# Kernel optimization log

Hardware: AMD Instinct MI355X
Metric: run time of the kernel (lower is better)

The kernel has to match this reference:

```python
import jax, jax.numpy as jnp
import numpy as np

TOKENS, D_MODEL, VOCAB = 8192, 1024, 32000


def setup_inputs() -> dict:
    key = jax.random.key(0)
    k1, k2, k3 = jax.random.split(key, 3)
    inp = jax.random.normal(k1, (TOKENS, D_MODEL), dtype=jnp.float32)
    proj_weight = jax.random.normal(k2, (VOCAB, D_MODEL), dtype=jnp.float32) * 0.02
    target = jax.random.randint(k3, (TOKENS,), 0, VOCAB, dtype=jnp.int64)
    return {"input": inp, "proj_weight": proj_weight, "target": target}


def reference(input, proj_weight, target):
    # Fused linear -> log_softmax -> NLL with reduction='sum'.
    # Original tiles over tokens/vocab with an online max/sum; the math is
    # exactly: loss = sum_t ( logsumexp_v(logits[t, :]) - logits[t, target[t]] )
    # with max/sum/target-score reductions done in float32 (fp_max/fp_sum/fp_target=True).
    logits = jnp.matmul(input, proj_weight.T).astype(jnp.float32)  # [tokens, vocab]
    lse = jax.nn.logsumexp(logits, axis=1)                          # [tokens]
    target_score = jnp.take_along_axis(logits, target[:, None].astype(jnp.int32), axis=1)[:, 0]
    return jnp.sum(lse - target_score)  # scalar, reduction='sum'
```

## Files before the change

kernel.cpp:

```cpp
#include <hip/hip_runtime.h>
#include <stdint.h>


#define TOKENS 8192
#define DMODEL 1024
#define VOCAB  32000

#define NBM32  (TOKENS / 128)
#define NBN32  (VOCAB / 256)
#define NWG32  (NBM32 * NBN32)

#define NBM    (TOKENS / 128)
#define NBN    (VOCAB / 128)
#define NWG    (NBM * NBN)
#define CHUNK  (NWG / 8)

typedef float  f32x4   __attribute__((ext_vector_type(4)));
typedef float  f32x16  __attribute__((ext_vector_type(16)));
typedef int    i32x8   __attribute__((ext_vector_type(8)));
typedef __bf16 bf16x8  __attribute__((ext_vector_type(8)));
typedef unsigned short u16;
typedef u16 u16x4 __attribute__((ext_vector_type(4)));

__device__ __forceinline__ u16 f2bf(float f) {
  union { float f; uint32_t u; } v; v.f = f;
  return (u16)((v.u + 0x7FFFu + ((v.u >> 16) & 1u)) >> 16);
}

__device__ __forceinline__ uint8_t f2e4m3(float x) {
  union { float f; uint32_t u; } v; v.f = x;
  const uint32_t s = (v.u >> 24) & 0x80u;
  const float ax = fabsf(x);
  if (ax >= 464.f) return (uint8_t)(s | 0x7E);
  if (ax < 0.015625f) {
    const int q = (int)rintf(ax * 512.f);
    return (uint8_t)(s | (uint32_t)q);
  }
  uint32_t u = v.u;
  u += 0x000FFFFFu + ((u >> 20) & 1u);
  const int E = (int)((u >> 23) & 0xFF) - 127;
  const uint32_t m3 = (u >> 20) & 0x7u;
  return (uint8_t)(s | (uint32_t)(((E + 7) << 3) | m3));
}

__device__ __forceinline__ void g2lds16(const void* gsrc, void* ldst) {
  __builtin_amdgcn_global_load_lds(
      (const __attribute__((address_space(1))) uint32_t*)(uintptr_t)gsrc,
      (__attribute__((address_space(3))) uint32_t*)(uintptr_t)ldst,
      16, 0, 0);
}

__global__ void convert_fp8_tiled(const float* __restrict__ in, uint8_t* __restrict__ out,
                                  long long total, int NR, int log2ts, float scale) {
  const long long step = (long long)gridDim.x * blockDim.x * 8;
  for (long long d = ((long long)blockIdx.x * blockDim.x + threadIdx.x) * 8;
       d < total; d += step) {
    const long long tile = d >> log2ts;
    const int x  = (int)(d & ((1 << log2ts) - 1));
    const int sub = x >> 11;
    const int l   = (x >> 5) & 63;
    const int b0  = x & 31;
    const int rb  = (int)(tile >> 4);
    const int kt  = (int)(tile & 15);
    const int row = rb * NR + sub * 32 + (l & 31);
    const int k   = kt * 64 + (l >> 5) * 32 + b0;
    const float* src = in + (size_t)row * DMODEL + k;
    const float4 f0 = *(const float4*)src;
    const float4 f1 = *(const float4*)(src + 4);
    uint8_t r[8] = { f2e4m3(f0.x * scale), f2e4m3(f0.y * scale),
                     f2e4m3(f0.z * scale), f2e4m3(f0.w * scale),
                     f2e4m3(f1.x * scale), f2e4m3(f1.y * scale),
                     f2e4m3(f1.z * scale), f2e4m3(f1.w * scale) };
    *(uint64_t*)(out + d) = *(const uint64_t*)r;
  }
}

template <int NCHUNK>
__device__ __forceinline__ void stage_lin(const uint8_t* __restrict__ src, uint8_t* dst,
                                          int wave, int lane) {
#pragma unroll
  for (int p = 0; p < NCHUNK / 4; ++p) {
    const int c = p * 4 + wave;
    g2lds16(src + c * 1024 + lane * 16, (void*)(dst + c * 1024));
  }
}

__device__ __forceinline__ void kstep32(const uint8_t* As, const uint8_t* Bs,
                                        f32x16 (&acc)[2][4],
                                        int wr, int wc, int lane) {
  i32x8 a[2], b[4];
  const uint8_t* ap = As + (wr * 2) * 2048 + lane * 32;
#pragma unroll
  for (int mi = 0; mi < 2; ++mi) {
    *(uint4*)&a[mi]       = *(const uint4*)(ap + mi * 2048);
    *((uint4*)&a[mi] + 1) = *(const uint4*)(ap + mi * 2048 + 16);
  }
  const uint8_t* bp = Bs + (wc * 4) * 2048 + lane * 32;
#pragma unroll
  for (int ni = 0; ni < 4; ++ni) {
    *(uint4*)&b[ni]       = *(const uint4*)(bp + ni * 2048);
    *((uint4*)&b[ni] + 1) = *(const uint4*)(bp + ni * 2048 + 16);
  }
  __builtin_amdgcn_s_setprio(1);
#pragma unroll
  for (int mi = 0; mi < 2; ++mi)
#pragma unroll
    for (int ni = 0; ni < 4; ++ni)
      acc[mi][ni] = __builtin_amdgcn_mfma_scale_f32_32x32x64_f8f6f4(
          a[mi], b[ni], acc[mi][ni], 0, 0,
          0, 0x7F7F7F7F, 0, 0x7F7F7F7F);
  __builtin_amdgcn_s_setprio(0);
}

__global__ __launch_bounds__(256, 2)
void gemm_lse_fp8v2(const uint8_t* __restrict__ A8, const uint8_t* __restrict__ B8,
                    float* __restrict__ S) {
  __shared__ uint8_t smem[49152];
  uint8_t* A0 = smem;
  uint8_t* B0 = smem + 8192;
  uint8_t* A1 = smem + 24576;
  uint8_t* B1 = smem + 32768;

  const int tid  = threadIdx.x;
  const int lane = tid & 63;
  const int wave = tid >> 6;
  const int wr = wave >> 1, wc = wave & 1;

  const int lid  = blockIdx.x;
  const int band = lid & 7;
  const int idx2 = lid >> 3;
  const int bn   = idx2 >> 3;
  const int bm   = band * 8 + (idx2 & 7);
  const int arow = bm * 128;

  const uint8_t* Abase = A8 + (size_t)(bm * 16) * 8192;
  const uint8_t* Bbase = B8 + (size_t)(bn * 16) * 16384;

  f32x16 acc[2][4];
#pragma unroll
  for (int mi = 0; mi < 2; ++mi)
#pragma unroll
    for (int ni = 0; ni < 4; ++ni) acc[mi][ni] = (f32x16)(0.f);

  stage_lin<8>(Abase, A0, wave, lane);
  stage_lin<16>(Bbase, B0, wave, lane);

#pragma unroll 1
  for (int tt = 0; tt < 8; ++tt) {
    const int t0 = 2 * tt;
    __syncthreads();
    if (t0 + 1 < 16) {
      stage_lin<8>(Abase + (size_t)(t0 + 1) * 8192, A1, wave, lane);
      stage_lin<16>(Bbase + (size_t)(t0 + 1) * 16384, B1, wave, lane);
    }
    kstep32(A0, B0, acc, wr, wc, lane);
    __syncthreads();
    if (t0 + 2 < 16) {
      stage_lin<8>(Abase + (size_t)(t0 + 2) * 8192, A0, wave, lane);
      stage_lin<16>(Bbase + (size_t)(t0 + 2) * 16384, B0, wave, lane);
    }
    kstep32(A1, B1, acc, wr, wc, lane);
  }

#pragma unroll
  for (int mi = 0; mi < 2; ++mi) {
#pragma unroll
    for (int r = 0; r < 16; ++r) {
      float v = 0.f;
#pragma unroll
      for (int ni = 0; ni < 4; ++ni) v += __expf(acc[mi][ni][r] * 0.0625f);
      v += __shfl_xor(v, 1);
      v += __shfl_xor(v, 2);
      v += __shfl_xor(v, 4);
      v += __shfl_xor(v, 8);
      v += __shfl_xor(v, 16);
      if ((lane & 31) == 0) {
        const int row = arow + (wr * 2 + mi) * 32 + (r & 3) + 8 * (r >> 2) + 4 * (lane >> 5);
        atomicAdd(&S[row], v);
      }
    }
  }
}

__global__ __launch_bounds__(256)
void gemm_lse_fb(const float* __restrict__ Af, const float* __restrict__ Bf,
                 float* __restrict__ S) {
  __shared__ u16 As[128 * 64];
  __shared__ u16 Bs[128 * 64];

  const int tid  = threadIdx.x;
  const int lane = tid & 63;
  const int wave = tid >> 6;
  const int wr = wave >> 1, wc = wave & 1;
  const int l15 = lane & 15, l4 = lane >> 4;

  const int lid = blockIdx.x;
  const int wid = (lid & 7) * CHUNK + (lid >> 3);
  const int bm = wid & (NBM - 1);
  const int bn = wid / NBM;

  f32x4 acc[4][4];
#pragma unroll
  for (int m = 0; m < 4; ++m)
#pragma unroll
    for (int n = 0; n < 4; ++n) acc[m][n] = (f32x4)(0.f);

  for (int kt = 0; kt < DMODEL / 64; ++kt) {
    const int k0 = kt * 64;
    {
      const int row = tid >> 4;
      const int kq  = (tid & 15) * 4;
#pragma unroll
      for (int r = 0; r < 8; ++r) {
        const int rr = r * 16 + row;
        const int kd = kq ^ ((rr & 7) << 3);
        float4 a4 = *(const float4*)(Af + (size_t)(bm * 128 + rr) * DMODEL + k0 + kq);
        float4 b4 = *(const float4*)(Bf + (size_t)(bn * 128 + rr) * DMODEL + k0 + kq);
        u16x4 ap = { f2bf(a4.x), f2bf(a4.y), f2bf(a4.z), f2bf(a4.w) };
        u16x4 bp = { f2bf(b4.x), f2bf(b4.y), f2bf(b4.z), f2bf(b4.w) };
        *(u16x4*)&As[rr * 64 + kd] = ap;
        *(u16x4*)&Bs[rr * 64 + kd] = bp;
      }
    }
    __syncthreads();
#pragma unroll
    for (int kk = 0; kk < 2; ++kk) {
      bf16x8 av[4], bv[4];
      const int swz = (l15 & 7) << 3;
      const int kc  = (kk * 32 + l4 * 8) ^ swz;
#pragma unroll
      for (int m = 0; m < 4; ++m)
        av[m] = *(const bf16x8*)&As[(wr * 64 + m * 16 + l15) * 64 + kc];
#pragma unroll
      for (int n = 0; n < 4; ++n)
        bv[n] = *(const bf16x8*)&Bs[(wc * 64 + n * 16 + l15) * 64 + kc];
#pragma unroll
      for (int m = 0; m < 4; ++m)
#pragma unroll
        for (int n = 0; n < 4; ++n)
          acc[m][n] = __builtin_amdgcn_mfma_f32_16x16x32_bf16(av[m], bv[n], acc[m][n], 0, 0, 0);
    }
    __syncthreads();
  }

#pragma unroll
  for (int m = 0; m < 4; ++m) {
#pragma unroll
    for (int j = 0; j < 4; ++j) {
      float v = 0.f;
#pragma unroll
      for (int n = 0; n < 4; ++n) v += __expf(acc[m][n][j]);
      v += __shfl_xor(v, 1);
      v += __shfl_xor(v, 2);
      v += __shfl_xor(v, 4);
      v += __shfl_xor(v, 8);
      if (l15 == 0) {
        const int row = bm * 128 + wr * 64 + m * 16 + l4 * 4 + j;
        atomicAdd(&S[row], v);
      }
    }
  }
}

__global__ void target_score_k(const float* __restrict__ inp, const float* __restrict__ W,
                               const int* __restrict__ tgt, float* __restrict__ ts) {
  const int gtid = blockIdx.x * blockDim.x + threadIdx.x;
  const int t = gtid >> 6;
  const int lane = threadIdx.x & 63;
  if (t >= TOKENS) return;
  bool allhi0 = true, anylo = false;
  for (int i = 0; i < 64; ++i) {
    if (tgt[2 * i + 1] != 0) allhi0 = false;
    if (tgt[2 * i] != 0) anylo = true;
  }
  const int v = (allhi0 && anylo) ? tgt[2 * t] : tgt[t];
  const float4* xr = (const float4*)(inp + (size_t)t * DMODEL);
  const float4* wr = (const float4*)(W + (size_t)v * DMODEL);
  float s = 0.f;
#pragma unroll
  for (int i = 0; i < 4; ++i) {
    float4 a = xr[lane + 64 * i];
    float4 b = wr[lane + 64 * i];
    s += a.x * b.x + a.y * b.y + a.z * b.z + a.w * b.w;
  }
#pragma unroll
  for (int off = 32; off >= 1; off >>= 1) s += __shfl_xor(s, off);
  if (lane == 0) ts[t] = s;
}

__global__ void finalize_k(const float* __restrict__ S, const float* __restrict__ ts,
                           float* __restrict__ out) {
  __shared__ float red[16];
  float s = 0.f;
  for (int t = threadIdx.x; t < TOKENS; t += blockDim.x) s += __logf(S[t]) - ts[t];
#pragma unroll
  for (int off = 32; off >= 1; off >>= 1) s += __shfl_xor(s, off);
  const int wave = threadIdx.x >> 6, lane = threadIdx.x & 63;
  if (lane == 0) red[wave] = s;
  __syncthreads();
  if (threadIdx.x == 0) {
    float tot = 0.f;
    for (int w = 0; w < (int)(blockDim.x >> 6); ++w) tot += red[w];
    out[0] = tot;
  }
}

extern "C" void kernel_launch(void* const* d_in, const int* in_sizes, int n_in,
                              void* d_out, int out_size, void* d_ws, size_t ws_size,
                              hipStream_t stream) {
  const float* inp = (const float*)d_in[0];
  const float* W   = (const float*)d_in[1];
  const int*   tgt = (const int*)d_in[2];
  float* out = (float*)d_out;

  char* ws = (char*)d_ws;
  float* S  = (float*)ws;
  float* ts = (float*)(ws + 32 * 1024);
  const size_t offA = 64 * 1024;
  const long long totalA = (long long)TOKENS * DMODEL;
  const long long totalB = (long long)VOCAB * DMODEL;
  const size_t offB = offA + (size_t)totalA;
  const size_t need = offB + (size_t)totalB;
  const bool preconv = ws_size >= need;

  hipMemsetAsync(S, 0, TOKENS * sizeof(float), stream);

  if (preconv) {
    uint8_t* A8 = (uint8_t*)(ws + offA);
    uint8_t* B8 = (uint8_t*)(ws + offB);
    convert_fp8_tiled<<<4096, 256, 0, stream>>>(inp, A8, totalA, 128, 13, 1.0f);
    convert_fp8_tiled<<<16000, 256, 0, stream>>>(W, B8, totalB, 256, 14, 16.0f);
    gemm_lse_fp8v2<<<NWG32, 256, 0, stream>>>(A8, B8, S);
  } else {
    gemm_lse_fb<<<NWG, 256, 0, stream>>>(inp, W, S);
  }
  target_score_k<<<(TOKENS * 64) / 256, 256, 0, stream>>>(inp, W, tgt, ts);
  finalize_k<<<1, 1024, 0, stream>>>(S, ts, out);
}
```

Measured before the change: 376.2 us.

## Load FP8 MFMA operands directly from global into registers, dropping LDS staging

Replaces the LDS double-buffered staging in the FP8 GEMM+LSE kernel with per-wave direct global loads into register double buffers, removing all __syncthreads. The conversion kernel now uses a single 128-row tile layout for both operands, so each wave reads its B slice as a contiguous 128-row block. This removes LDS traffic and barrier costs but loses cross-wave sharing of A/B tiles, so each wave fetches its operands from global/L2 separately, raising cache bandwidth demand.

New measurement: 532.6 us. 41.6% more time.

```diff
diff --git a/kernel.cpp b/kernel.cpp
--- a/kernel.cpp
+++ b/kernel.cpp
@@ -6,9 +6,9 @@
 #define DMODEL 1024
 #define VOCAB  32000
 
-#define NBM32  (TOKENS / 128)
-#define NBN32  (VOCAB / 256)
-#define NWG32  (NBM32 * NBN32)
+#define NBMF   (TOKENS / 128)
+#define NBNF   (VOCAB / 256)
+#define NWGF   (NBMF * NBNF)
 
 #define NBM    (TOKENS / 128)
 #define NBN    (VOCAB / 128)
@@ -43,27 +43,20 @@
   return (uint8_t)(s | (uint32_t)(((E + 7) << 3) | m3));
 }
 
-__device__ __forceinline__ void g2lds16(const void* gsrc, void* ldst) {
-  __builtin_amdgcn_global_load_lds(
-      (const __attribute__((address_space(1))) uint32_t*)(uintptr_t)gsrc,
-      (__attribute__((address_space(3))) uint32_t*)(uintptr_t)ldst,
-      16, 0, 0);
-}
-
 __global__ void convert_fp8_tiled(const float* __restrict__ in, uint8_t* __restrict__ out,
-                                  long long total, int NR, int log2ts, float scale) {
+                                  long long total, float scale) {
   const long long step = (long long)gridDim.x * blockDim.x * 8;
   for (long long d = ((long long)blockIdx.x * blockDim.x + threadIdx.x) * 8;
        d < total; d += step) {
-    const long long tile = d >> log2ts;
-    const int x  = (int)(d & ((1 << log2ts) - 1));
+    const long long tile = d >> 13;
+    const int x   = (int)(d & 8191);
     const int sub = x >> 11;
-    const int l   = (x >> 5) & 63;
-    const int b0  = x & 31;
+    const int rem = x & 2047;
+    const int l   = rem >> 5;
     const int rb  = (int)(tile >> 4);
     const int kt  = (int)(tile & 15);
-    const int row = rb * NR + sub * 32 + (l & 31);
-    const int k   = kt * 64 + (l >> 5) * 32 + b0;
+    const int row = rb * 128 + sub * 32 + (l & 31);
+    const int k   = kt * 64 + (l >> 5) * 32 + (rem & 31);
     const float* src = in + (size_t)row * DMODEL + k;
     const float4 f0 = *(const float4*)src;
     const float4 f1 = *(const float4*)(src + 4);
@@ -75,55 +68,11 @@
   }
 }
 
-template <int NCHUNK>
-__device__ __forceinline__ void stage_lin(const uint8_t* __restrict__ src, uint8_t* dst,
-                                          int wave, int lane) {
-#pragma unroll
-  for (int p = 0; p < NCHUNK / 4; ++p) {
-    const int c = p * 4 + wave;
-    g2lds16(src + c * 1024 + lane * 16, (void*)(dst + c * 1024));
-  }
-}
-
-__device__ __forceinline__ void kstep32(const uint8_t* As, const uint8_t* Bs,
-                                        f32x16 (&acc)[2][4],
-                                        int wr, int wc, int lane) {
-  i32x8 a[2], b[4];
-  const uint8_t* ap = As + (wr * 2) * 2048 + lane * 32;
-#pragma unroll
-  for (int mi = 0; mi < 2; ++mi) {
-    *(uint4*)&a[mi]       = *(const uint4*)(ap + mi * 2048);
-    *((uint4*)&a[mi] + 1) = *(const uint4*)(ap + mi * 2048 + 16);
-  }
-  const uint8_t* bp = Bs + (wc * 4) * 2048 + lane * 32;
-#pragma unroll
-  for (int ni = 0; ni < 4; ++ni) {
-    *(uint4*)&b[ni]       = *(const uint4*)(bp + ni * 2048);
-    *((uint4*)&b[ni] + 1) = *(const uint4*)(bp + ni * 2048 + 16);
-  }
-  __builtin_amdgcn_s_setprio(1);
-#pragma unroll
-  for (int mi = 0; mi < 2; ++mi)
-#pragma unroll
-    for (int ni = 0; ni < 4; ++ni)
-      acc[mi][ni] = __builtin_amdgcn_mfma_scale_f32_32x32x64_f8f6f4(
-          a[mi], b[ni], acc[mi][ni], 0, 0,
-          0, 0x7F7F7F7F, 0, 0x7F7F7F7F);
-  __builtin_amdgcn_s_setprio(0);
-}
-
-__global__ __launch_bounds__(256, 2)
-void gemm_lse_fp8v2(const uint8_t* __restrict__ A8, const uint8_t* __restrict__ B8,
-                    float* __restrict__ S) {
-  __shared__ uint8_t smem[49152];
-  uint8_t* A0 = smem;
-  uint8_t* B0 = smem + 8192;
-  uint8_t* A1 = smem + 24576;
-  uint8_t* B1 = smem + 32768;
-
-  const int tid  = threadIdx.x;
-  const int lane = tid & 63;
-  const int wave = tid >> 6;
+__global__ __launch_bounds__(256)
+void gemm_lse_flat(const uint8_t* __restrict__ A8, const uint8_t* __restrict__ B8,
+                   float* __restrict__ S) {
+  const int lane = threadIdx.x & 63;
+  const int wave = threadIdx.x >> 6;
   const int wr = wave >> 1, wc = wave & 1;
 
   const int lid  = blockIdx.x;
@@ -133,8 +82,8 @@
   const int bm   = band * 8 + (idx2 & 7);
   const int arow = bm * 128;
 
-  const uint8_t* Abase = A8 + (size_t)(bm * 16) * 8192;
-  const uint8_t* Bbase = B8 + (size_t)(bn * 16) * 16384;
+  const uint8_t* Abase = A8 + (size_t)(bm * 16) * 8192 + (wr * 2) * 2048 + lane * 32;
+  const uint8_t* Bbase = B8 + (size_t)((2 * bn + wc) * 16) * 8192 + lane * 32;
 
   f32x16 acc[2][4];
 #pragma unroll
@@ -142,25 +91,44 @@
 #pragma unroll
     for (int ni = 0; ni < 4; ++ni) acc[mi][ni] = (f32x16)(0.f);
 
-  stage_lin<8>(Abase, A0, wave, lane);
-  stage_lin<16>(Bbase, B0, wave, lane);
-
+  i32x8 a0[2], b0[4], a1[2], b1[4];
+
+#define LOAD_A(dst, t)                                                    \
+  _Pragma("unroll")                                                       \
+  for (int mi = 0; mi < 2; ++mi)                                          \
+    dst[mi] = *(const i32x8*)(Abase + (size_t)(t) * 8192 + mi * 2048);
+#define LOAD_B(dst, t)                                                    \
+  _Pragma("unroll")                                                       \
+  for (int ni = 0; ni < 4; ++ni)                                          \
+    dst[ni] = *(const i32x8*)(Bbase + (size_t)(t) * 8192 + ni * 2048);
+#define COMPUTE(a, b)                                                     \
+  __builtin_amdgcn_s_setprio(1);                                          \
+  _Pragma("unroll")                                                       \
+  for (int mi = 0; mi < 2; ++mi) {                                        \
+    _Pragma("unroll")                                                     \
+    for (int ni = 0; ni < 4; ++ni)                                        \
+      acc[mi][ni] = __builtin_amdgcn_mfma_scale_f32_32x32x64_f8f6f4(      \
+          a[mi], b[ni], acc[mi][ni], 0, 0,                                \
+          0, 0x7F7F7F7F, 0, 0x7F7F7F7F);                                  \
+  }                                                                       \
+  __builtin_amdgcn_s_setprio(0);
+
+  LOAD_A(a0, 0)
+  LOAD_B(b0, 0)
 #pragma unroll 1
-  for (int tt = 0; tt < 8; ++tt) {
-    const int t0 = 2 * tt;
-    __syncthreads();
-    if (t0 + 1 < 16) {
-      stage_lin<8>(Abase + (size_t)(t0 + 1) * 8192, A1, wave, lane);
-      stage_lin<16>(Bbase + (size_t)(t0 + 1) * 16384, B1, wave, lane);
-    }
-    kstep32(A0, B0, acc, wr, wc, lane);
-    __syncthreads();
-    if (t0 + 2 < 16) {
-      stage_lin<8>(Abase + (size_t)(t0 + 2) * 8192, A0, wave, lane);
-      stage_lin<16>(Bbase + (size_t)(t0 + 2) * 16384, B0, wave, lane);
-    }
-    kstep32(A1, B1, acc, wr, wc, lane);
-  }
+  for (int t = 0; t < 16; t += 2) {
+    LOAD_A(a1, t + 1)
+    LOAD_B(b1, t + 1)
+    COMPUTE(a0, b0)
+    if (t + 2 < 16) {
+      LOAD_A(a0, t + 2)
+      LOAD_B(b0, t + 2)
+    }
+    COMPUTE(a1, b1)
+  }
+#undef LOAD_A
+#undef LOAD_B
+#undef COMPUTE
 
 #pragma unroll
   for (int mi = 0; mi < 2; ++mi) {
@@ -175,7 +143,7 @@
       v += __shfl_xor(v, 8);
       v += __shfl_xor(v, 16);
       if ((lane & 31) == 0) {
-        const int row = arow + (wr * 2 + mi) * 32 + (r & 3) + 8 * (r >> 2) + 4 * (lane >> 5);
+        const int row = arow + wr * 64 + mi * 32 + (r & 3) + 8 * (r >> 2) + 4 * (lane >> 5);
         atomicAdd(&S[row], v);
       }
     }
@@ -328,9 +296,9 @@
   if (preconv) {
     uint8_t* A8 = (uint8_t*)(ws + offA);
     uint8_t* B8 = (uint8_t*)(ws + offB);
-    convert_fp8_tiled<<<4096, 256, 0, stream>>>(inp, A8, totalA, 128, 13, 1.0f);
-    convert_fp8_tiled<<<16000, 256, 0, stream>>>(W, B8, totalB, 256, 14, 16.0f);
-    gemm_lse_fp8v2<<<NWG32, 256, 0, stream>>>(A8, B8, S);
+    convert_fp8_tiled<<<4096, 256, 0, stream>>>(inp, A8, totalA, 1.0f);
+    convert_fp8_tiled<<<16000, 256, 0, stream>>>(W, B8, totalB, 16.0f);
+    gemm_lse_flat<<<NWGF, 256, 0, stream>>>(A8, B8, S);
   } else {
     gemm_lse_fb<<<NWG, 256, 0, stream>>>(inp, W, S);
   }
```
